# Performance work log

Hardware: AMD Instinct MI355X
Metric: run time of the kernel (lower is better)

## Reference

```python
import jax, jax.numpy as jnp
import numpy as np

LRELU = 0.2
BN_EPS = 1e-5
SN_EPS = 1e-12


def _spectral_norm(w, u):
    # One power iteration (torch train-mode behavior), u/v detached.
    wm = w.reshape(w.shape[0], -1)            # [out, in*kh*kw]
    u = jax.lax.stop_gradient(u)
    v = wm.T @ u
    v = v / (jnp.linalg.norm(v) + SN_EPS)
    u2 = wm @ v
    u2 = u2 / (jnp.linalg.norm(u2) + SN_EPS)
    sigma = u2 @ (wm @ v)
    return w / sigma


def _conv(x, w):
    # Conv2d kernel=4, stride=2, padding=1, no bias
    return jax.lax.conv_general_dilated(
        x, w, window_strides=(2, 2), padding=((1, 1), (1, 1)),
        dimension_numbers=("NCHW", "OIHW", "NCHW"))


def _bn(x, g, b):
    # BatchNorm2d in training mode: biased batch stats over (N,H,W)
    m = x.mean(axis=(0, 2, 3), keepdims=True)
    v = x.var(axis=(0, 2, 3), keepdims=True)
    xh = (x - m) * jax.lax.rsqrt(v + BN_EPS)
    return xh * g[None, :, None, None] + b[None, :, None, None]


def _lrelu(x):
    return jnp.where(x >= 0, x, LRELU * x)


def setup_inputs() -> dict:
    key = jax.random.key(0)
    ks = jax.random.split(key, 16)
    ndf, nc, oc, N = 64, 3, 64, 64
    chans = [(nc, ndf), (ndf, ndf * 2), (ndf * 2, ndf * 4),
             (ndf * 4, ndf * 4), (ndf * 4, ndf * 8), (ndf * 8, oc)]
    inp = {"image": jax.random.normal(ks[0], (N, nc, 128, 128), jnp.float32)}
    for i, (ci, co) in enumerate(chans):
        inp[f"w{i+1}"] = 0.02 * jax.random.normal(ks[1 + i], (co, ci, 4, 4), jnp.float32)
        inp[f"u{i+1}"] = jax.random.normal(ks[7 + i], (co,), jnp.float32)
    for i, c in enumerate([ndf * 2, ndf * 4, ndf * 4, ndf * 8]):
        inp[f"g{i+1}"] = jnp.ones((c,), jnp.float32)
        inp[f"b{i+1}"] = jnp.zeros((c,), jnp.float32)
    A, B, C = oc * 2 * 2, oc, ndf  # 256, 64, 64
    stddev = 1.0 / A
    inp["T"] = jax.random.uniform(ks[13], (A, B, C), jnp.float32,
                                  minval=stddev, maxval=1.0)
    return inp


def reference(image, w1, w2, w3, w4, w5, w6, u1, u2, u3, u4, u5, u6,
              g1, b1, g2, b2, g3, b3, g4, b4, T):
    x = _lrelu(_conv(image, _spectral_norm(w1, u1)))
    x = _lrelu(_bn(_conv(x, _spectral_norm(w2, u2)), g1, b1))
    x = _lrelu(_bn(_conv(x, _spectral_norm(w3, u3)), g2, b2))
    x = _lrelu(_bn(_conv(x, _spectral_norm(w4, u4)), g3, b3))
    x = _lrelu(_bn(_conv(x, _spectral_norm(w5, u5)), g4, b4))
    x = _conv(x, _spectral_norm(w6, u6))          # [N, 64, 2, 2]; Dropout2d(p=0) = identity
    A, Bo, C = T.shape
    flat = x.reshape(-1, A)                        # [N, 256]
    Ms = (flat @ T.reshape(A, Bo * C)).reshape(-1, Bo, C)   # [N, B, C]
    # MiniBatchDiscrimination: out[i,b] = sum_j exp(-||Ms[i,b]-Ms[j,b]||_1)
    d = jnp.abs(Ms[:, None, :, :] - Ms[None, :, :, :]).sum(-1)  # [N, N, B]
    mbd = jnp.exp(-d).sum(axis=1)                  # [N, B]
    return jnp.concatenate([flat, mbd], axis=1)    # [N, 320]
```

## Files before the change

### kernel.cpp

```cpp
#include <hip/hip_runtime.h>
#include <hip/hip_bf16.h>
#include <math.h>

#define LRELU 0.2f
#define BN_EPS 1e-5f
#define SN_EPS 1e-12f

typedef __attribute__((ext_vector_type(4))) float f32x4;
typedef __attribute__((ext_vector_type(8))) short bf16x8;
typedef __attribute__((ext_vector_type(4))) short bf16x4;

__device__ inline float bf2f(short s) {
  union { unsigned u; float f; } c; c.u = ((unsigned)(unsigned short)s) << 16; return c.f;
}
__device__ inline short f2bf(float f) {
  __hip_bfloat16 h = __float2bfloat16(f); return *(short*)&h;
}

__device__ inline int xcd_swz(int bx, int nwg) {
  int chunk = nwg >> 3;
  return (bx & 7) * chunk + (bx >> 3);
}

__device__ inline float blockReduceSum256(float v, volatile float* red) {
  #pragma unroll
  for (int o = 32; o > 0; o >>= 1) v += __shfl_down(v, o, 64);
  const int tid = threadIdx.x;
  __syncthreads();
  if ((tid & 63) == 0) red[tid >> 6] = v;
  __syncthreads();
  return red[0] + red[1] + red[2] + red[3];
}

struct SNArgs {
  const float* w[6];
  const float* u[6];
  int outc[6];
  int ink[6];
};

__global__ __launch_bounds__(256) void sn_v(SNArgs args, float* __restrict__ vpart) {
  const int l = blockIdx.z;
  const int in_k = args.ink[l], out_c = args.outc[l];
  const int tid = threadIdx.x;
  const int j = blockIdx.x * 256 + tid;
  if (blockIdx.x * 256 >= in_k) return;
  const int rows = out_c >> 3;
  const int i0 = blockIdx.y * rows;
  __shared__ float uS[64];
  if (tid < rows) uS[tid] = args.u[l][i0 + tid];
  __syncthreads();
  if (j >= in_k) return;
  const float* __restrict__ w = args.w[l] + (size_t)i0 * in_k;
  float t = 0.f;
  for (int i = 0; i < rows; ++i) t = fmaf(w[(size_t)i * in_k + j], uS[i], t);
  vpart[((size_t)(l * 8 + blockIdx.y)) * 8192 + j] = t;
}

__global__ __launch_bounds__(256) void sn_v_red(SNArgs args, const float* __restrict__ vpart,
                                                float* __restrict__ vbuf, float* __restrict__ pA) {
  const int l = blockIdx.y;
  const int in_k = args.ink[l];
  const int tid = threadIdx.x;
  const int j = blockIdx.x * 256 + tid;
  __shared__ float red[4];
  float s = 0.f;
  if (j < in_k) {
    #pragma unroll
    for (int ch = 0; ch < 8; ++ch)
      s += vpart[((size_t)(l * 8 + ch)) * 8192 + j];
    vbuf[l * 8192 + j] = s;
  }
  const float bs = blockReduceSum256((j < in_k) ? s * s : 0.f, red);
  if (tid == 0) pA[l * 32 + blockIdx.x] = bs;
}

__global__ __launch_bounds__(64) void sn_norm1(SNArgs args, const float* __restrict__ pA,
                                               float* __restrict__ rinv) {
  const int l = blockIdx.x;
  if (threadIdx.x != 0) return;
  const int nb = (args.ink[l] + 255) >> 8;
  float s = 0.f;
  for (int b = 0; b < nb; ++b) s += pA[l * 32 + b];
  rinv[l] = 1.f / (sqrtf(s) + SN_EPS);
}

__global__ __launch_bounds__(256) void sn_t2(SNArgs args, const float* __restrict__ vbuf,
                                             const float* __restrict__ rinv,
                                             float* __restrict__ pB) {
  const int l = blockIdx.y;
  const int in_k = args.ink[l], out_c = args.outc[l];
  const int lane = threadIdx.x & 63, wv = threadIdx.x >> 6;
  const int row = blockIdx.x * 4 + wv;
  __shared__ float red[4];
  float sq = 0.f;
  if (row < out_c) {
    const float* __restrict__ wr = args.w[l] + (size_t)row * in_k;
    const float* __restrict__ v = vbuf + l * 8192;
    float a0 = 0.f, a1 = 0.f, a2 = 0.f, a3 = 0.f;
    for (int j = lane * 4; j < in_k; j += 256) {
      f32x4 w4 = *(const f32x4*)(wr + j);
      f32x4 v4 = *(const f32x4*)(v + j);
      a0 = fmaf(w4[0], v4[0], a0);
      a1 = fmaf(w4[1], v4[1], a1);
      a2 = fmaf(w4[2], v4[2], a2);
      a3 = fmaf(w4[3], v4[3], a3);
    }
    float t = (a0 + a1) + (a2 + a3);
    #pragma unroll
    for (int o = 32; o > 0; o >>= 1) t += __shfl_down(t, o, 64);
    if (lane == 0) { t *= rinv[l]; sq = t * t; }
  }
  __syncthreads();
  if (lane == 0) red[wv] = sq;
  __syncthreads();
  if (threadIdx.x == 0) pB[l * 128 + blockIdx.x] = red[0] + red[1] + red[2] + red[3];
}

__global__ __launch_bounds__(64) void sn_norm2(const float* __restrict__ pB,
                                               float* __restrict__ inv_sigma) {
  const int l = blockIdx.x;
  if (threadIdx.x != 0) return;
  float s = 0.f;
  for (int b = 0; b < 128; ++b) s += pB[l * 128 + b];
  const float n2 = sqrtf(s);
  const float sigma = s / (n2 + SN_EPS);
  inv_sigma[l] = 1.f / sigma;
}

__global__ __launch_bounds__(256) void zero_pads(__hip_bfloat16* r0, __hip_bfloat16* r1) {
  int t = blockIdx.x * 256 + threadIdx.x;
  if (t < 2048) {
    r0[16777216 + t] = __float2bfloat16(0.f);
    r1[16777216 + t] = __float2bfloat16(0.f);
  }
}

struct PPArgs {
  const float* w[6];
  __hip_bfloat16* dst[6];
  int cinr[6];
  int cout[6];
  int kpad[6];
  int kreal[6];
};

__global__ __launch_bounds__(256) void prepack_all(PPArgs args, const float* __restrict__ invs) {
  const int l = blockIdx.y;
  int e = blockIdx.x * 256 + threadIdx.x;
  const int total = args.kpad[l] * args.cout[l];
  if (e >= total) return;
  const int CINR = args.cinr[l], COUT = args.cout[l], KREAL = args.kreal[l];
  int j = e & 7, lane = (e >> 3) & 63, frag = e >> 9;
  int nfrags = COUT >> 4;
  int ks = frag / nfrags, nf = frag - ks * nfrags;
  int k = ks * 32 + ((lane >> 4) << 3) + j;
  int co = (nf << 4) + (lane & 15);
  float val = 0.f;
  if (k < KREAL) {
    int khw = k / CINR, ci = k - khw * CINR;
    int kh = khw >> 2, kw = khw & 3;
    val = args.w[l][(((size_t)co * CINR + ci) * 4 + kh) * 4 + kw] * invs[l];
  }
  args.dst[l][e] = __float2bfloat16(val);
}

__global__ __launch_bounds__(256) void im2col_l1(const float* __restrict__ img,
                                                 __hip_bfloat16* __restrict__ a2) {
  int t = blockIdx.x * 256 + threadIdx.x;
  int c = t & 7;
  int m = t >> 3;
  int n = m >> 12;
  int hw = m & 4095;
  int ho = hw >> 6, wo = hw & 63;
  int ihb = 2 * ho - 1, iwb = 2 * wo - 1;
  const float* __restrict__ ib = img + (size_t)n * 49152;
  short vals[8];
  #pragma unroll
  for (int j = 0; j < 8; ++j) {
    int k = c * 8 + j;
    float val = 0.f;
    if (k < 48) {
      int khw = k / 3;
      int ci = k - khw * 3;
      int kh = khw >> 2, kw = khw & 3;
      int ih = ihb + kh, iw = iwb + kw;
      if (((unsigned)ih < 128u) & ((unsigned)iw < 128u))
        val = ib[ci * 16384 + ih * 128 + iw];
    }
    vals[j] = f2bf(val);
  }
  *(bf16x8*)(a2 + (size_t)m * 64 + c * 8) = *(bf16x8*)vals;
}

template<int CIN, int COUT, int MF, bool FUSE>
__global__ __launch_bounds__(256) void conv_mfma(
    const __hip_bfloat16* __restrict__ x,
    const __hip_bfloat16* __restrict__ wf,
    __hip_bfloat16* __restrict__ out)
{
  constexpr int CB = CIN / 32;

  const int bx = xcd_swz(blockIdx.x, gridDim.x);
  const int lane = threadIdx.x & 63;
  const int wid  = threadIdx.x >> 6;
  const int wm = wid >> 1, wn = wid & 1;
  const int mbase = bx * (MF * 32) + wm * (MF * 16);
  const int cobase = blockIdx.y * 64 + wn * 32;

  int offm[MF];
  #pragma unroll
  for (int mf = 0; mf < MF; ++mf) {
    int m = mbase + mf * 16 + (lane & 15);
    offm[mf] = m * CIN;
  }
  const int koff = (lane >> 4) << 3;
  const __hip_bfloat16* wfp = wf + ((size_t)((blockIdx.y * 4 + wn * 2) * 64 + lane)) * 8;

  f32x4 acc[MF][2];
  #pragma unroll
  for (int mf = 0; mf < MF; ++mf) {
    acc[mf][0] = (f32x4){0.f, 0.f, 0.f, 0.f};
    acc[mf][1] = (f32x4){0.f, 0.f, 0.f, 0.f};
  }

  #pragma unroll
  for (int cb = 0; cb < CB; ++cb) {
    bf16x8 a[MF], b[2];
    #pragma unroll
    for (int mf = 0; mf < MF; ++mf) a[mf] = *(const bf16x8*)(x + offm[mf] + koff + cb * 32);
    #pragma unroll
    for (int nf = 0; nf < 2; ++nf)
      b[nf] = *(const bf16x8*)(wfp + (size_t)cb * (COUT * 32) + nf * 512);
    #pragma unroll
    for (int mf = 0; mf < MF; ++mf)
      #pragma unroll
      for (int nf = 0; nf < 2; ++nf)
        acc[mf][nf] = __builtin_amdgcn_mfma_f32_16x16x32_bf16(a[mf], b[nf], acc[mf][nf], 0, 0, 0);
  }

  const int r0 = (lane >> 4) * 4;
  const int cw = cobase + (lane & 15);
  #pragma unroll
  for (int mf = 0; mf < MF; ++mf)
    #pragma unroll
    for (int nf = 0; nf < 2; ++nf)
      #pragma unroll
      for (int r = 0; r < 4; ++r) {
        float v = acc[mf][nf][r];
        if (FUSE) v = (v >= 0.f) ? v : LRELU * v;
        int m = mbase + mf * 16 + r0 + r;
        out[(size_t)m * COUT + (cw + nf * 16)] = __float2bfloat16(v);
      }
}

template<int CIN, int COUT, int HIN, int HOUT, int Z, bool SPLITK, bool BNIN, bool BF16P>
__global__ __launch_bounds__(256) void conv_mfma4(
    const __hip_bfloat16* __restrict__ x,
    const __hip_bfloat16* __restrict__ wf,
    const float* __restrict__ sbp,
    __hip_bfloat16* __restrict__ outb, float* __restrict__ outp)
{
  constexpr int WIN = HIN, WO = HOUT;
  constexpr int CB = CIN / 32;
  constexpr int KHW_PER = 16 / Z;
  constexpr int PADOFF = 16777216;
  constexpr int M = 64 * HOUT * WO;

  const int bx = xcd_swz(blockIdx.x, gridDim.x);
  const int lane = threadIdx.x & 63;
  const int wid  = threadIdx.x >> 6;
  const int wm = wid >> 1, wn = wid & 1;
  const int mbase = bx * 128 + wm * 64;
  const int nbase = blockIdx.y * 128 + wn * 64;
  const int khw0 = blockIdx.z * KHW_PER;

  int offm[4], ihb[4], iwb[4];
  #pragma unroll
  for (int mf = 0; mf < 4; ++mf) {
    int m = mbase + mf * 16 + (lane & 15);
    int n = m / (HOUT * WO);
    int hw = m - n * (HOUT * WO);
    int ho = hw / WO, wo = hw - ho * WO;
    ihb[mf] = 2 * ho - 1;
    iwb[mf] = 2 * wo - 1;
    offm[mf] = ((n * HIN + ihb[mf]) * WIN + iwb[mf]) * CIN;
  }
  const int koff = (lane >> 4) << 3;
  const __hip_bfloat16* wfp = wf + ((size_t)((nbase >> 4) * 64 + lane)) * 8;

  f32x4 acc[4][4];
  #pragma unroll
  for (int mf = 0; mf < 4; ++mf)
    #pragma unroll
    for (int nf = 0; nf < 4; ++nf) acc[mf][nf] = (f32x4){0.f, 0.f, 0.f, 0.f};

  #pragma unroll
  for (int cb = 0; cb < CB; ++cb) {
    f32x4 s0, s1, o0, o1;
    if (BNIN) {
      const int cbase = cb * 32 + koff;
      s0 = *(const f32x4*)(sbp + cbase);
      s1 = *(const f32x4*)(sbp + cbase + 4);
      o0 = *(const f32x4*)(sbp + CIN + cbase);
      o1 = *(const f32x4*)(sbp + CIN + cbase + 4);
    }
    #pragma unroll
    for (int ki = 0; ki < KHW_PER; ++ki) {
      const int khw = khw0 + ki;
      const int kh = khw >> 2, kw = khw & 3;
      bf16x8 a[4], b[4];
      bool vm[4];
      #pragma unroll
      for (int mf = 0; mf < 4; ++mf) {
        int ih = ihb[mf] + kh, iw = iwb[mf] + kw;
        vm[mf] = ((unsigned)ih < (unsigned)HIN) & ((unsigned)iw < (unsigned)WIN);
        int off = vm[mf] ? (offm[mf] + (kh * WIN + kw) * CIN + koff + cb * 32)
                         : (PADOFF + koff + cb * 32);
        a[mf] = *(const bf16x8*)(x + off);
      }
      const size_t ks = (size_t)khw * CB + cb;
      #pragma unroll
      for (int nf = 0; nf < 4; ++nf)
        b[nf] = *(const bf16x8*)(wfp + ks * (COUT * 32) + nf * 512);
      if (BNIN) {
        #pragma unroll
        for (int mf = 0; mf < 4; ++mf) {
          bf16x8 t = a[mf];
          #pragma unroll
          for (int j = 0; j < 8; ++j) {
            float fv = bf2f(t[j]);
            float sc = (j < 4) ? s0[j] : s1[j - 4];
            float of = (j < 4) ? o0[j] : o1[j - 4];
            fv = fmaf(fv, sc, of);
            fv = fmaxf(fv, LRELU * fv);
            t[j] = vm[mf] ? f2bf(fv) : (short)0;
          }
          a[mf] = t;
        }
      }
      #pragma unroll
      for (int mf = 0; mf < 4; ++mf)
        #pragma unroll
        for (int nf = 0; nf < 4; ++nf)
          acc[mf][nf] = __builtin_amdgcn_mfma_f32_16x16x32_bf16(a[mf], b[nf], acc[mf][nf], 0, 0, 0);
    }
  }

  const int r0 = (lane >> 4) * 4;
  const int cw = nbase + (lane & 15);
  #pragma unroll
  for (int mf = 0; mf < 4; ++mf)
    #pragma unroll
    for (int nf = 0; nf < 4; ++nf)
      #pragma unroll
      for (int r = 0; r < 4; ++r) {
        const int m = mbase + mf * 16 + r0 + r;
        const int co = cw + nf * 16;
        if (SPLITK) {
          if (BF16P)
            outb[(size_t)blockIdx.z * M * COUT + (size_t)m * COUT + co] = __float2bfloat16(acc[mf][nf][r]);
          else
            outp[(size_t)blockIdx.z * M * COUT + (size_t)m * COUT + co] = acc[mf][nf][r];
        } else {
          outb[(size_t)m * COUT + co] = __float2bfloat16(acc[mf][nf][r]);
        }
      }
}

template<int Z, int MCHUNKS, bool BF16P>
__global__ __launch_bounds__(256) void sk_bn_fuse(const float* __restrict__ partf,
                                                  const __hip_bfloat16* __restrict__ partb,
                                                  __hip_bfloat16* __restrict__ xo,
                                                  float* __restrict__ statp, int M, int C) {
  const int chunk = blockIdx.x;
  const int c0 = blockIdx.y * 64 + (threadIdx.x & 7) * 8;
  const int mrow = threadIdx.x >> 3;
  const int rows = M / MCHUNKS;
  const size_t MC = (size_t)M * C;
  float s[8], s2[8];
  #pragma unroll
  for (int j = 0; j < 8; ++j) { s[j] = 0.f; s2[j] = 0.f; }
  for (int mi = mrow; mi < rows; mi += 32) {
    const int m = chunk * rows + mi;
    const size_t base = (size_t)m * C + c0;
    float av[8];
    if (BF16P) {
      bf16x8 v0 = *(const bf16x8*)(partb + base);
      #pragma unroll
      for (int j = 0; j < 8; ++j) av[j] = bf2f(v0[j]);
      #pragma unroll
      for (int z = 1; z < Z; ++z) {
        bf16x8 vz = *(const bf16x8*)(partb + (size_t)z * MC + base);
        #pragma unroll
        for (int j = 0; j < 8; ++j) av[j] += bf2f(vz[j]);
      }
    } else {
      f32x4 a = *(const f32x4*)(partf + base);
      f32x4 b = *(const f32x4*)(partf + base + 4);
      #pragma unroll
      for (int z = 1; z < Z; ++z) {
        a += *(const f32x4*)(partf + (size_t)z * MC + base);
        b += *(const f32x4*)(partf + (size_t)z * MC + base + 4);
      }
      #pragma unroll
      for (int j = 0; j < 4; ++j) { av[j] = a[j]; av[4 + j] = b[j]; }
    }
    bf16x8 o;
    #pragma unroll
    for (int j = 0; j < 8; ++j) {
      o[j] = f2bf(av[j]);
      s[j] += av[j];
      s2[j] = fmaf(av[j], av[j], s2[j]);
    }
    *(bf16x8*)(xo + base) = o;
  }
  __shared__ float ls[8][256], ls2[8][256];
  const int t = threadIdx.x;
  #pragma unroll
  for (int j = 0; j < 8; ++j) { ls[j][t] = s[j]; ls2[j][t] = s2[j]; }
  __syncthreads();
  #pragma unroll
  for (int off = 16; off >= 1; off >>= 1) {
    if (mrow < off) {
      #pragma unroll
      for (int j = 0; j < 8; ++j) {
        ls[j][t]  += ls[j][t + off * 8];
        ls2[j][t] += ls2[j][t + off * 8];
      }
    }
    __syncthreads();
  }
  if (t < 8) {
    #pragma unroll
    for (int j = 0; j < 8; ++j) {
      statp[(size_t)chunk * C + c0 + j] = ls[j][t];
      statp[(size_t)(MCHUNKS + chunk) * C + c0 + j] = ls2[j][t];
    }
  }
}

__global__ __launch_bounds__(256) void conv_l6_mfma(
    const __hip_bfloat16* __restrict__ x,
    const __hip_bfloat16* __restrict__ wf,
    float* __restrict__ x6, float* __restrict__ out)
{
  constexpr int CIN = 512, COUT = 64, HIN = 4;
  constexpr int CB = CIN / 32;
  constexpr int PADOFF = 16777216;

  const int lane = threadIdx.x & 63;
  const int wid  = threadIdx.x >> 6;
  const int wm = wid >> 1, wn = wid & 1;
  const int mbase = blockIdx.x * 32 + wm * 16;

  int m0 = mbase + (lane & 15);
  int n = m0 >> 2;
  int hw = m0 & 3;
  int ho = hw >> 1, wo = hw & 1;
  int ihb = 2 * ho - 1;
  int iwb = 2 * wo - 1;
  int offm = ((n * HIN + ihb) * HIN + iwb) * CIN;

  const int koff = (lane >> 4) << 3;
  const __hip_bfloat16* wfp = wf + ((size_t)((wn * 2) * 64 + lane)) * 8;

  f32x4 acc[2];
  acc[0] = (f32x4){0.f, 0.f, 0.f, 0.f};
  acc[1] = (f32x4){0.f, 0.f, 0.f, 0.f};

  #pragma unroll
  for (int khw = 0; khw < 16; ++khw) {
    const int kh = khw >> 2, kw = khw & 3;
    const int ih = ihb + kh, iw = iwb + kw;
    const bool v = ((unsigned)ih < (unsigned)HIN) & ((unsigned)iw < (unsigned)HIN);
    const int off = v ? (offm + (kh * HIN + kw) * CIN + koff) : (PADOFF + koff);
    const __hip_bfloat16* ap = x + off;
    #pragma unroll
    for (int cb = 0; cb < CB; ++cb) {
      const int ks = khw * CB + cb;
      bf16x8 a = *(const bf16x8*)(ap + cb * 32);
      bf16x8 b0 = *(const bf16x8*)(wfp + (size_t)ks * (COUT * 32));
      bf16x8 b1 = *(const bf16x8*)(wfp + (size_t)ks * (COUT * 32) + 512);
      acc[0] = __builtin_amdgcn_mfma_f32_16x16x32_bf16(a, b0, acc[0], 0, 0, 0);
      acc[1] = __builtin_amdgcn_mfma_f32_16x16x32_bf16(a, b1, acc[1], 0, 0, 0);
    }
  }

  const int r0 = (lane >> 4) * 4;
  const int cw = wn * 32 + (lane & 15);
  #pragma unroll
  for (int nf = 0; nf < 2; ++nf)
    #pragma unroll
    for (int r = 0; r < 4; ++r) {
      int m = mbase + r0 + r;
      int nn = m >> 2, p = m & 3;
      float v = acc[nf][r];
      x6[(size_t)nn * 256 + (cw + nf * 16) * 4 + p] = v;
      out[(size_t)nn * 320 + (cw + nf * 16) * 4 + p] = v;
    }
}

template<int MCHUNKS>
__global__ __launch_bounds__(256) void bn_stats_a(const __hip_bfloat16* __restrict__ x,
                                                  float* __restrict__ part, int M, int C) {
  const int chunk = blockIdx.x;
  const int c0 = blockIdx.y * 64 + (threadIdx.x & 7) * 8;
  const int mrow = threadIdx.x >> 3;
  const int rows = M / MCHUNKS;
  float s[8], s2[8];
  #pragma unroll
  for (int j = 0; j < 8; ++j) { s[j] = 0.f; s2[j] = 0.f; }
  for (int mi = mrow; mi < rows; mi += 32) {
    const int m = chunk * rows + mi;
    bf16x8 v = *(const bf16x8*)(x + (size_t)m * C + c0);
    #pragma unroll
    for (int j = 0; j < 8; ++j) {
      float f = bf2f(v[j]);
      s[j] += f;
      s2[j] = fmaf(f, f, s2[j]);
    }
  }
  __shared__ float ls[8][256], ls2[8][256];
  const int t = threadIdx.x;
  #pragma unroll
  for (int j = 0; j < 8; ++j) { ls[j][t] = s[j]; ls2[j][t] = s2[j]; }
  __syncthreads();
  #pragma unroll
  for (int off = 16; off >= 1; off >>= 1) {
    if (mrow < off) {
      #pragma unroll
      for (int j = 0; j < 8; ++j) {
        ls[j][t]  += ls[j][t + off * 8];
        ls2[j][t] += ls2[j][t + off * 8];
      }
    }
    __syncthreads();
  }
  if (t < 8) {
    #pragma unroll
    for (int j = 0; j < 8; ++j) {
      part[(size_t)chunk * C + c0 + j] = ls[j][t];
      part[(size_t)(MCHUNKS + chunk) * C + c0 + j] = ls2[j][t];
    }
  }
}

template<int MCHUNKS>
__global__ __launch_bounds__(64) void bn_stats_b(const float* __restrict__ part,
                                                 const float* __restrict__ g,
                                                 const float* __restrict__ b,
                                                 float* __restrict__ sb, int M, int C) {
  int c = blockIdx.x * 64 + threadIdx.x;
  float s = 0.f, s2 = 0.f;
  for (int ch = 0; ch < MCHUNKS; ++ch) {
    s  += part[(size_t)ch * C + c];
    s2 += part[(size_t)(MCHUNKS + ch) * C + c];
  }
  float invM = 1.f / (float)M;
  float mean = s * invM;
  float var = s2 * invM - mean * mean;
  float scale = g[c] * rsqrtf(var + BN_EPS);
  sb[c] = scale;
  sb[C + c] = b[c] - mean * scale;
}

__global__ __launch_bounds__(256) void bn_apply(__hip_bfloat16* __restrict__ x,
                                                const float* __restrict__ sb,
                                                int C, int nvec) {
  int idx = blockIdx.x * 256 + threadIdx.x;
  if (idx >= nvec) return;
  size_t e = (size_t)idx * 8;
  int c0 = (int)(e % (size_t)C);
  bf16x8 v = *(bf16x8*)(x + e);
  bf16x8 o;
  #pragma unroll
  for (int j = 0; j < 8; ++j) {
    int c = c0 + j;
    float f = bf2f(v[j]);
    f = fmaf(f, sb[c], sb[C + c]);
    f = (f >= 0.f) ? f : LRELU * f;
    o[j] = f2bf(f);
  }
  *(bf16x8*)(x + e) = o;
}

__global__ __launch_bounds__(256) void ms_kernel(const float* __restrict__ x6,
                                                 const float* __restrict__ T,
                                                 float* __restrict__ Ms) {
  const int cb = blockIdx.x;
  const int nb = blockIdx.y;
  const int c  = threadIdx.x & 63;
  const int ns = threadIdx.x >> 6;
  __shared__ float fsh[16][256];
  for (int t = threadIdx.x; t < 4096; t += 256) {
    int n = t >> 8, a = t & 255;
    fsh[n][a] = x6[(size_t)(nb * 16 + n) * 256 + a];
  }
  __syncthreads();
  const int col = cb * 64 + c;
  float acc0 = 0.f, acc1 = 0.f, acc2 = 0.f, acc3 = 0.f;
  #pragma unroll 8
  for (int a = 0; a < 256; ++a) {
    float tv = T[(size_t)a * 4096 + col];
    acc0 = fmaf(fsh[ns * 4 + 0][a], tv, acc0);
    acc1 = fmaf(fsh[ns * 4 + 1][a], tv, acc1);
    acc2 = fmaf(fsh[ns * 4 + 2][a], tv, acc2);
    acc3 = fmaf(fsh[ns * 4 + 3][a], tv, acc3);
  }
  const int nbase = nb * 16 + ns * 4;
  Ms[(size_t)(nbase + 0) * 4096 + col] = acc0;
  Ms[(size_t)(nbase + 1) * 4096 + col] = acc1;
  Ms[(size_t)(nbase + 2) * 4096 + col] = acc2;
  Ms[(size_t)(nbase + 3) * 4096 + col] = acc3;
}

__global__ __launch_bounds__(256) void mbd_kernel(const float* __restrict__ Ms,
                                                  float* __restrict__ out) {
  const int b  = blockIdx.x;
  const int ib = blockIdx.y;
  const int tid = threadIdx.x;
  __shared__ float Mb[64][65];
  for (int idx = tid; idx < 4096; idx += 256) {
    const int i = idx >> 6, cc = idx & 63;
    Mb[i][cc] = Ms[(size_t)i * 4096 + b * 64 + cc];
  }
  __syncthreads();
  const int i  = ib * 16 + (tid >> 4);
  const int jg = tid & 15;
  float ssum = 0.f;
  for (int j = jg; j < 64; j += 16) {
    float d = 0.f;
    #pragma unroll
    for (int cc = 0; cc < 64; ++cc) d += fabsf(Mb[i][cc] - Mb[j][cc]);
    ssum += expf(-d);
  }
  ssum += __shfl_xor(ssum, 1, 64);
  ssum += __shfl_xor(ssum, 2, 64);
  ssum += __shfl_xor(ssum, 4, 64);
  ssum += __shfl_xor(ssum, 8, 64);
  if (jg == 0) out[(size_t)i * 320 + 256 + b] = ssum;
}

extern "C" void kernel_launch(void* const* d_in, const int* in_sizes, int n_in,
                              void* d_out, int out_size, void* d_ws, size_t ws_size,
                              hipStream_t stream) {
  const float* image = (const float*)d_in[0];
  const float* W[6] = {(const float*)d_in[1], (const float*)d_in[3], (const float*)d_in[5],
                       (const float*)d_in[7], (const float*)d_in[9], (const float*)d_in[11]};
  const float* U[6] = {(const float*)d_in[2], (const float*)d_in[4], (const float*)d_in[6],
                       (const float*)d_in[8], (const float*)d_in[10], (const float*)d_in[12]};
  const float* G[4] = {(const float*)d_in[13], (const float*)d_in[15],
                       (const float*)d_in[17], (const float*)d_in[19]};
  const float* Bb[4] = {(const float*)d_in[14], (const float*)d_in[16],
                        (const float*)d_in[18], (const float*)d_in[20]};
  const float* T = (const float*)d_in[21];
  float* out = (float*)d_out;

  float* f = (float*)d_ws;
  float* inv_sigma = f;
  float* part      = f + 1024;
  float* x6        = f + 1024 + 65536 + 1024;
  float* Ms        = f + 1024 + 65536 + 1024 + 16384;
  float* vbuf      = f + 360448;
  float* pA        = f + 360448 + 49152;
  float* pB        = pA + 256;
  float* rinv      = pB + 768;
  float* sbL[4];
  for (int i = 0; i < 4; ++i) sbL[i] = f + 412672 + i * 2048;
  __hip_bfloat16* bfb = (__hip_bfloat16*)(f + 524288);
  const size_t REGION = 16777216 + 2048;
  __hip_bfloat16* region0 = bfb;
  __hip_bfloat16* region1 = region0 + REGION;
  __hip_bfloat16* wf1 = region1 + REGION;
  __hip_bfloat16* wf2 = wf1 + 4096;
  __hip_bfloat16* wf3 = wf2 + 131072;
  __hip_bfloat16* wf4 = wf3 + 524288;
  __hip_bfloat16* wf5 = wf4 + 1048576;
  __hip_bfloat16* wf6 = wf5 + 2097152;
  float* skpart = (float*)(wf6 + 524288);
  __hip_bfloat16* skpartb = (__hip_bfloat16*)skpart;
  float* vpart  = skpart + 8388608;

  __hip_bfloat16* a2col = region0;
  __hip_bfloat16* x1 = region1;
  __hip_bfloat16* x2 = region0;
  __hip_bfloat16* x3 = region1;
  __hip_bfloat16* x4 = region0;
  __hip_bfloat16* x5 = region1;

  zero_pads<<<8, 256, 0, stream>>>(region0, region1);

  SNArgs sa;
  const int outc[6] = {64, 128, 256, 256, 512, 64};
  const int ink[6]  = {48, 1024, 2048, 4096, 4096, 8192};
  for (int l = 0; l < 6; ++l) { sa.w[l] = W[l]; sa.u[l] = U[l]; sa.outc[l] = outc[l]; sa.ink[l] = ink[l]; }

  sn_v<<<dim3(32, 8, 6), 256, 0, stream>>>(sa, vpart);
  sn_v_red<<<dim3(32, 6), 256, 0, stream>>>(sa, vpart, vbuf, pA);
  sn_norm1<<<6, 64, 0, stream>>>(sa, pA, rinv);
  sn_t2<<<dim3(128, 6), 256, 0, stream>>>(sa, vbuf, rinv, pB);
  sn_norm2<<<6, 64, 0, stream>>>(pB, inv_sigma);

  PPArgs pa;
  __hip_bfloat16* wfp_[6] = {wf1, wf2, wf3, wf4, wf5, wf6};
  const int cinr_[6]  = {3, 64, 128, 256, 256, 512};
  const int kpad_[6]  = {64, 1024, 2048, 4096, 4096, 8192};
  const int kreal_[6] = {48, 1024, 2048, 4096, 4096, 8192};
  for (int l = 0; l < 6; ++l) {
    pa.w[l] = W[l]; pa.dst[l] = wfp_[l]; pa.cinr[l] = cinr_[l];
    pa.cout[l] = outc[l]; pa.kpad[l] = kpad_[l]; pa.kreal[l] = kreal_[l];
  }
  prepack_all<<<dim3(8192, 6), 256, 0, stream>>>(pa, inv_sigma);

  im2col_l1<<<8192, 256, 0, stream>>>(image, a2col);

  conv_mfma<64, 64, 4, true><<<dim3(2048, 1), 256, 0, stream>>>(a2col, wf1, x1);

  conv_mfma4<64, 128, 64, 32, 1, false, false, false><<<dim3(512, 1, 1), 256, 0, stream>>>(x1, wf2, nullptr, x2, nullptr);
  bn_stats_a<256><<<dim3(256, 2), 256, 0, stream>>>(x2, part, 65536, 128);
  bn_stats_b<256><<<2, 64, 0, stream>>>(part, G[0], Bb[0], sbL[0], 65536, 128);

  conv_mfma4<128, 256, 32, 16, 2, true, true, true><<<dim3(128, 2, 2), 256, 0, stream>>>(x2, wf3, sbL[0], skpartb, nullptr);
  sk_bn_fuse<2, 128, true><<<dim3(128, 4), 256, 0, stream>>>(nullptr, skpartb, x3, part, 16384, 256);
  bn_stats_b<128><<<4, 64, 0, stream>>>(part, G[1], Bb[1], sbL[1], 16384, 256);

  conv_mfma4<256, 256, 16, 8, 8, true, true, true><<<dim3(32, 2, 8), 256, 0, stream>>>(x3, wf4, sbL[1], skpartb, nullptr);
  sk_bn_fuse<8, 128, true><<<dim3(128, 4), 256, 0, stream>>>(nullptr, skpartb, x4, part, 4096, 256);
  bn_stats_b<128><<<4, 64, 0, stream>>>(part, G[2], Bb[2], sbL[2], 4096, 256);

  conv_mfma4<256, 512, 8, 4, 16, true, true, true><<<dim3(8, 4, 16), 256, 0, stream>>>(x4, wf5, sbL[2], skpartb, nullptr);
  sk_bn_fuse<16, 32, true><<<dim3(32, 8), 256, 0, stream>>>(nullptr, skpartb, x5, part, 1024, 512);
  bn_stats_b<32><<<8, 64, 0, stream>>>(part, G[3], Bb[3], sbL[3], 1024, 512);

  bn_apply<<<256, 256, 0, stream>>>(x5, sbL[3], 512, 65536);
  conv_l6_mfma<<<8, 256, 0, stream>>>(x5, wf6, x6, out);

  ms_kernel<<<dim3(64, 4), 256, 0, stream>>>(x6, T, Ms);
  mbd_kernel<<<dim3(64, 4), 256, 0, stream>>>(Ms, out);
}
```

Before: 357.3 us.

## Stage layer-2 conv tiles through LDS with register prefetch

Adds a conv_lds kernel for layer 2 that cooperatively loads the 128x32 activation tile and the 128-channel weight slab into shared memory each K step. Waves then read their MFMA fragments from LDS, so each global element is loaded once per block rather than separately by each wave. The next step's data is prefetched into registers while the current step computes. In exchange it needs two barriers per K step and extra LDS traffic, and possible bank conflicts on the fragment reads.

After: 344.3 us. -3.6%, faster.

```diff
diff --git a/kernel.cpp b/kernel.cpp
--- a/kernel.cpp
+++ b/kernel.cpp
@@ -254,6 +254,109 @@
       }
 }
 
+template<int CIN, int COUT, int HIN, int HOUT>
+__global__ __launch_bounds__(256) void conv_lds(
+    const __hip_bfloat16* __restrict__ x,
+    const __hip_bfloat16* __restrict__ wf,
+    __hip_bfloat16* __restrict__ outb)
+{
+  constexpr int WIN = HIN, WO = HOUT;
+  constexpr int CB = CIN / 32;
+  constexpr int NSTEP = 16 * CB;
+  constexpr int PADOFF = 16777216;
+
+  __shared__ __hip_bfloat16 As[128 * 32];
+  __shared__ __hip_bfloat16 Bs[4096];
+
+  const int bx = xcd_swz(blockIdx.x, gridDim.x);
+  const int t = threadIdx.x;
+  const int lane = t & 63;
+  const int wid = t >> 6;
+  const int wm = wid >> 1, wn = wid & 1;
+  const int mbase = bx * 128;
+  const int nbase = blockIdx.y * 128;
+
+  const int sr0 = t >> 2;
+  const int sl  = t & 3;
+  int rowbase[2], ihbs[2], iwbs[2];
+  #pragma unroll
+  for (int i = 0; i < 2; ++i) {
+    int m = mbase + sr0 + i * 64;
+    int n = m / (HOUT * WO);
+    int hw = m - n * (HOUT * WO);
+    int ho = hw / WO, wo = hw - ho * WO;
+    ihbs[i] = 2 * ho - 1;
+    iwbs[i] = 2 * wo - 1;
+    rowbase[i] = ((n * HIN + ihbs[i]) * WIN + iwbs[i]) * CIN;
+  }
+  const size_t bslab0 = (size_t)(nbase >> 4) * 512 + (size_t)t * 8;
+
+  f32x4 acc[4][4];
+  #pragma unroll
+  for (int mf = 0; mf < 4; ++mf)
+    #pragma unroll
+    for (int nf = 0; nf < 4; ++nf) acc[mf][nf] = (f32x4){0.f, 0.f, 0.f, 0.f};
+
+  bf16x8 ra0, ra1, rb0, rb1;
+  auto load_step = [&](int ks) {
+    const int khw = ks / CB, cb = ks - khw * CB;
+    const int kh = khw >> 2, kw = khw & 3;
+    const int kbyteoff = cb * 32 + sl * 8;
+    {
+      int ih = ihbs[0] + kh, iw = iwbs[0] + kw;
+      bool v = ((unsigned)ih < (unsigned)HIN) & ((unsigned)iw < (unsigned)WIN);
+      int off = v ? (rowbase[0] + (kh * WIN + kw) * CIN + kbyteoff) : PADOFF;
+      ra0 = *(const bf16x8*)(x + off);
+    }
+    {
+      int ih = ihbs[1] + kh, iw = iwbs[1] + kw;
+      bool v = ((unsigned)ih < (unsigned)HIN) & ((unsigned)iw < (unsigned)WIN);
+      int off = v ? (rowbase[1] + (kh * WIN + kw) * CIN + kbyteoff) : PADOFF;
+      ra1 = *(const bf16x8*)(x + off);
+    }
+    const size_t bo = (size_t)ks * (COUT * 32) + bslab0;
+    rb0 = *(const bf16x8*)(wf + bo);
+    rb1 = *(const bf16x8*)(wf + bo + 2048);
+  };
+
+  load_step(0);
+  for (int ks = 0; ks < NSTEP; ++ks) {
+    __syncthreads();
+    *(bf16x8*)(&As[sr0 * 32 + sl * 8]) = ra0;
+    *(bf16x8*)(&As[(sr0 + 64) * 32 + sl * 8]) = ra1;
+    *(bf16x8*)(&Bs[t * 8]) = rb0;
+    *(bf16x8*)(&Bs[2048 + t * 8]) = rb1;
+    __syncthreads();
+    if (ks + 1 < NSTEP) load_step(ks + 1);
+    bf16x8 af[4], bfr[4];
+    #pragma unroll
+    for (int mf = 0; mf < 4; ++mf) {
+      const int ra = wm * 64 + mf * 16 + (lane & 15);
+      af[mf] = *(const bf16x8*)(&As[ra * 32 + (lane >> 4) * 8]);
+    }
+    #pragma unroll
+    for (int nf = 0; nf < 4; ++nf)
+      bfr[nf] = *(const bf16x8*)(&Bs[(wn * 4 + nf) * 512 + lane * 8]);
+    #pragma unroll
+    for (int mf = 0; mf < 4; ++mf)
+      #pragma unroll
+      for (int nf = 0; nf < 4; ++nf)
+        acc[mf][nf] = __builtin_amdgcn_mfma_f32_16x16x32_bf16(af[mf], bfr[nf], acc[mf][nf], 0, 0, 0);
+  }
+
+  const int r0w = (lane >> 4) * 4;
+  const int cw = nbase + wn * 64 + (lane & 15);
+  #pragma unroll
+  for (int mf = 0; mf < 4; ++mf)
+    #pragma unroll
+    for (int nf = 0; nf < 4; ++nf)
+      #pragma unroll
+      for (int r = 0; r < 4; ++r) {
+        const int m = mbase + wm * 64 + mf * 16 + r0w + r;
+        outb[(size_t)m * COUT + (cw + nf * 16)] = __float2bfloat16(acc[mf][nf][r]);
+      }
+}
+
 template<int CIN, int COUT, int HIN, int HOUT, int Z, bool SPLITK, bool BNIN, bool BF16P>
 __global__ __launch_bounds__(256) void conv_mfma4(
     const __hip_bfloat16* __restrict__ x,
@@ -326,17 +429,17 @@
       if (BNIN) {
         #pragma unroll
         for (int mf = 0; mf < 4; ++mf) {
-          bf16x8 t = a[mf];
+          bf16x8 tt = a[mf];
           #pragma unroll
           for (int j = 0; j < 8; ++j) {
-            float fv = bf2f(t[j]);
+            float fv = bf2f(tt[j]);
             float sc = (j < 4) ? s0[j] : s1[j - 4];
             float of = (j < 4) ? o0[j] : o1[j - 4];
             fv = fmaf(fv, sc, of);
             fv = fmaxf(fv, LRELU * fv);
-            t[j] = vm[mf] ? f2bf(fv) : (short)0;
+            tt[j] = vm[mf] ? f2bf(fv) : (short)0;
           }
-          a[mf] = t;
+          a[mf] = tt;
         }
       }
       #pragma unroll
@@ -717,7 +820,7 @@
 
   conv_mfma<64, 64, 4, true><<<dim3(2048, 1), 256, 0, stream>>>(a2col, wf1, x1);
 
-  conv_mfma4<64, 128, 64, 32, 1, false, false, false><<<dim3(512, 1, 1), 256, 0, stream>>>(x1, wf2, nullptr, x2, nullptr);
+  conv_lds<64, 128, 64, 32><<<dim3(512, 1, 1), 256, 0, stream>>>(x1, wf2, x2);
   bn_stats_a<256><<<dim3(256, 2), 256, 0, stream>>>(x2, part, 65536, 128);
   bn_stats_b<256><<<2, 64, 0, stream>>>(part, G[0], Bb[0], sbL[0], 65536, 128);
 
```
